# Optimization experiments

Hardware: AMD Instinct MI355X
Metric: run time of the kernel (lower is better)

The kernel has to match this reference:

```python
import jax, jax.numpy as jnp
import numpy as np

C = 256   # embedding_dim
B = 16
N = 2048
BN_EPS = 1e-5


def _sa_params(key, c):
    ks = jax.random.split(key, 8)
    s = 1.0 / np.sqrt(c)
    return dict(
        Wq=jax.random.normal(ks[0], (c // 2, c), jnp.float32) * s,
        Wk=jax.random.normal(ks[1], (c // 2, c), jnp.float32) * s,
        Wv=jax.random.normal(ks[2], (c, c), jnp.float32) * s,
        bv=jax.random.normal(ks[3], (c,), jnp.float32) * 0.01,
        Wt=jax.random.normal(ks[4], (c, c), jnp.float32) * s,
        bt=jax.random.normal(ks[5], (c,), jnp.float32) * 0.01,
        gamma=jnp.ones((c,), jnp.float32),
        beta=jnp.zeros((c,), jnp.float32),
    )


def setup_inputs() -> dict:
    key = jax.random.key(0)
    kx, k1, k2 = jax.random.split(key, 3)
    inp = {"x": jax.random.normal(kx, (B, C, N), jnp.float32)}
    for tag, kk in (("1", k1), ("2", k2)):
        for name, v in _sa_params(kk, C).items():
            inp[name + tag] = v
    return inp


def _sa_layer(x, Wq, Wk, Wv, bv, Wt, bt, gamma, beta):
    # 1x1 conv == per-point linear: [B,C,N]
    x_q = jnp.einsum('oc,bcn->bno', Wq, x)            # [B,N,C/2]
    x_k = jnp.einsum('oc,bcn->bon', Wk, x)            # [B,C/2,N]
    x_v = jnp.einsum('oc,bcn->bon', Wv, x) + bv[None, :, None]
    energy = jnp.einsum('bnc,bcm->bnm', x_q, x_k)     # [B,N,N]
    attn = jax.nn.softmax(energy, axis=-1)
    # offset-attention column-wise L1 renorm
    attn = attn / (1e-9 + attn.sum(axis=1, keepdims=True))
    x_r = jnp.einsum('bcn,bnm->bcm', x_v, attn)       # [B,C,N]
    h = x - x_r
    h = jnp.einsum('oc,bcn->bon', Wt, h) + bt[None, :, None]
    # BatchNorm1d (training mode, biased var over batch+points per channel)
    mean = h.mean(axis=(0, 2), keepdims=True)
    var = jnp.mean((h - mean) ** 2, axis=(0, 2), keepdims=True)
    h = (h - mean) * jax.lax.rsqrt(var + BN_EPS)
    h = h * gamma[None, :, None] + beta[None, :, None]
    return x + jax.nn.relu(h)


def reference(x,
              Wq1, Wk1, Wv1, bv1, Wt1, bt1, gamma1, beta1,
              Wq2, Wk2, Wv2, bv2, Wt2, bt2, gamma2, beta2):
    x1 = _sa_layer(x, Wq1, Wk1, Wv1, bv1, Wt1, bt1, gamma1, beta1)
    x2 = _sa_layer(x1, Wq2, Wk2, Wv2, bv2, Wt2, bt2, gamma2, beta2)
    return jnp.concatenate((x1, x2), axis=1)          # [B,2C,N]
```

## Files before the change

### kernel.cpp

```cpp
#include <hip/hip_runtime.h>

#define DI __device__ __forceinline__

typedef _Float16 f16_t;
typedef _Float16 f16x8 __attribute__((ext_vector_type(8)));
typedef float    f32x4 __attribute__((ext_vector_type(4)));

static_assert(sizeof(f16x8) == 16, "f16x8 must be 16B");

#define B_  16
#define C_  256
#define CH_ 128
#define N_  2048

DI f32x4 fzero(){ f32x4 z = {0.f,0.f,0.f,0.f}; return z; }
DI f16x8 ldg8(const f16_t* p){ return *(const f16x8*)p; }
DI f32x4 mfma16(f16x8 a, f16x8 b, f32x4 c){
  return __builtin_amdgcn_mfma_f32_16x16x32_f16(a, b, c, 0, 0, 0);
}
DI void split2(float v, f16_t& hi, f16_t& lo){
  hi = (f16_t)v; lo = (f16_t)(v - (float)hi);
}
DI int swz_b(int i){ return ((i&7)<<1) | ((i>>3)&1); }

#define GLL16(src, dst) __builtin_amdgcn_global_load_lds( \
    (const __attribute__((address_space(1))) void*)(src), \
    (__attribute__((address_space(3))) void*)(dst), 16, 0, 0)

__global__ void k_wconv(const float* q1,const float* k1,const float* v1,const float* t1,
                        const float* q2,const float* k2,const float* v2,const float* t2,
                        f16_t* out){
  int i = blockIdx.x*256 + threadIdx.x;
  int l = (i >= 196608) ? 1 : 0;
  int r = i - l*196608;
  const float* s; long dbase;
  if(r < 32768){ s = l? q2:q1; dbase = 0; }
  else if(r < 65536){ r -= 32768; s = l? k2:k1; dbase = 65536; }
  else if(r < 131072){ r -= 65536; s = l? v2:v1; dbase = 131072; }
  else { r -= 131072; s = l? t2:t1; dbase = 262144; }
  int o = r >> 8, c = r & 255;
  float v = s[o*256 + c];
  f16_t hi, lo; split2(v, hi, lo);
  f16_t* d = out + (long)l*393216 + dbase + (long)o*512;
  d[c] = hi; d[c+256] = lo;
}

__global__ void k_transpose(const float* __restrict__ X, long bstride,
                            f16_t* __restrict__ XtS){
  int b = blockIdx.x, n0 = blockIdx.y*32, c0 = blockIdx.z*64;
  __shared__ float tl[32][65];
  int t = threadIdx.x;
  int nn = t & 31, cr = t >> 5;
  const float* src = X + (long)b*bstride + n0 + nn;
  #pragma unroll
  for(int i=0;i<8;i++){
    int cc = cr + i*8;
    tl[nn][cc] = src[(long)(c0+cc)*N_];
  }
  __syncthreads();
  int n2 = t >> 3, cq = (t & 7)*8;
  __align__(16) f16_t hi8[8], lo8[8];
  #pragma unroll
  for(int j=0;j<8;j++) split2(tl[n2][cq+j], hi8[j], lo8[j]);
  f16_t* dst = XtS + ((long)b*N_ + n0 + n2)*512 + c0 + cq;
  *(f16x8*)dst         = *(f16x8*)hi8;
  *(f16x8*)(dst + 256) = *(f16x8*)lo8;
}

template<int LGX, int SPLIT_OUT, int BIAS>
__global__ __launch_bounds__(256) void k_gemm3(
    const f16_t* __restrict__ A, long sA,
    const f16_t* __restrict__ Bt, long sB,
    f16_t* __restrict__ out, int ldo, long sO,
    const float* __restrict__ bias)
{
  int i = blockIdx.x;
  int b = swz_b(i);
  int r = i>>4;
  int m0 = (r & ((1<<LGX)-1))*64, n0 = (r >> LGX)*64;
  int t = threadIdx.x, w = t>>6, l = t&63, lr = l&15, lg = l>>4;
  const f16_t* Ab = A + (long)b*sA + (long)(m0 + w*16 + lr)*512;
  const f16_t* Bb = Bt + (long)b*sB;
  f32x4 acc[4];
  #pragma unroll
  for(int i2=0;i2<4;i2++) acc[i2] = fzero();
  for(int k=0;k<256;k+=32){
    f16x8 ah = ldg8(Ab + k + lg*8);
    f16x8 al = ldg8(Ab + 256 + k + lg*8);
    #pragma unroll
    for(int ns=0;ns<4;ns++){
      const f16_t* brow = Bb + (long)(n0 + ns*16 + lr)*512;
      f16x8 bh = ldg8(brow + k + lg*8);
      f16x8 bl = ldg8(brow + 256 + k + lg*8);
      acc[ns] = mfma16(ah, bh, acc[ns]);
      acc[ns] = mfma16(ah, bl, acc[ns]);
      acc[ns] = mfma16(al, bh, acc[ns]);
    }
  }
  f16_t* ob = out + (long)b*sO;
  #pragma unroll
  for(int ns=0;ns<4;ns++){
    #pragma unroll
    for(int j=0;j<4;j++){
      int row = m0 + w*16 + lg*4 + j;
      int col = n0 + ns*16 + lr;
      float v = acc[ns][j];
      if(BIAS) v += bias[row];
      if(SPLIT_OUT){
        f16_t hi, lo; split2(v, hi, lo);
        ob[(long)row*ldo + col]       = hi;
        ob[(long)row*ldo + col + 128] = lo;
      } else {
        ob[(long)row*ldo + col] = (f16_t)v;
      }
    }
  }
}

__global__ __launch_bounds__(256) void k_rowstats(
    const f16_t* __restrict__ xqS, const f16_t* __restrict__ xkS,
    float* __restrict__ rowoff)
{
  extern __shared__ __align__(16) char smem[];
  const int bi = blockIdx.x;
  const int b = swz_b(bi);
  const int n0 = (bi>>4)*64;
  const int t = threadIdx.x, w = t>>6, l = t&63, lr = l&15, lg = l>>4;

  const f16_t* qp = xqS + ((long)b*N_ + n0 + w*16 + lr)*256;
  f16x8 bqh[4], bql[4];
  #pragma unroll
  for(int k=0;k<4;k++){
    bqh[k] = ldg8(qp + k*32 + lg*8);
    bql[k] = ldg8(qp + 128 + k*32 + lg*8);
  }
  const f16_t* kb = xkS + (long)b*N_*256;

  const int krow_off = l>>5, kslot = l&31;
  #define KSTAGE(mm, buf) do {                                                \
    char* kd = smem + (buf)*16384;                                            \
    _Pragma("unroll")                                                         \
    for(int r=0;r<4;r++){                                                     \
      int row = (r*4+w)*2 + krow_off;                                         \
      const f16_t* ksrc = kb + (long)((mm) + row)*256 + ((kslot ^ (row&15))*8);\
      GLL16(ksrc, kd + (r*4+w)*1024);                                         \
    }                                                                         \
  } while(0)

  float rmax = -3e38f, rsum = 0.f;
  KSTAGE(0, 0);

  #pragma unroll 1
  for(int i=0; i<64; i++){
    const int cur = i&1, nxt = cur^1;
    const int mm = (i<63) ? (i+1)*32 : 0;
    KSTAGE(mm, nxt);
    asm volatile("s_waitcnt vmcnt(4)" ::: "memory");
    asm volatile("s_barrier" ::: "memory");
    const char* kbuf = smem + cur*16384;
    #pragma unroll
    for(int s=0;s<2;s++){
      const char* krow = kbuf + (s*16 + lr)*512;
      f16x8 ah[4], al_[4];
      #pragma unroll
      for(int k=0;k<4;k++){
        ah[k]  = *(const f16x8*)(krow + ((((4*k+lg) ^ lr))<<4));
        al_[k] = *(const f16x8*)(krow + ((16 + (((4*k+lg)) ^ lr))<<4));
      }
      f32x4 a1 = fzero(), a2 = fzero(), a3 = fzero();
      #pragma unroll
      for(int k=0;k<4;k++) a1 = mfma16(ah[k],  bqh[k], a1);
      #pragma unroll
      for(int k=0;k<4;k++) a2 = mfma16(ah[k],  bql[k], a2);
      #pragma unroll
      for(int k=0;k<4;k++) a3 = mfma16(al_[k], bqh[k], a3);
      f32x4 acc = (a1 + a2) + a3;
      float vm = fmaxf(fmaxf(acc[0],acc[1]), fmaxf(acc[2],acc[3]));
      float nm = fmaxf(rmax, vm);
      rsum = rsum*__expf(rmax-nm)
           + __expf(acc[0]-nm)+__expf(acc[1]-nm)+__expf(acc[2]-nm)+__expf(acc[3]-nm);
      rmax = nm;
    }
    asm volatile("s_barrier" ::: "memory");
  }
  #undef KSTAGE

  #pragma unroll
  for(int off=16; off<64; off<<=1){
    float om = __shfl_xor(rmax, off, 64);
    float os = __shfl_xor(rsum, off, 64);
    float nm = fmaxf(rmax, om);
    rsum = rsum*__expf(rmax-nm) + os*__expf(om-nm);
    rmax = nm;
  }
  if(lg==0) rowoff[(long)b*N_ + n0 + w*16 + lr] = rmax + __logf(rsum);
}

__global__ __launch_bounds__(256) void k_apply(
    const f16_t* __restrict__ xqS, const f16_t* __restrict__ xkS,
    const f16_t* __restrict__ xv, const float* __restrict__ rowoff,
    const float* __restrict__ X, long xbstride, f16_t* __restrict__ h0T)
{
  extern __shared__ __align__(16) char smem[];
  const int bi = blockIdx.x;
  const int b = swz_b(bi);
  const int m0 = (bi>>4)*64;
  const int t = threadIdx.x, w = t>>6, l = t&63, lr = l&15, lg = l>>4;
  float* ro_s = (float*)(smem + 65536);
  {
    const float* rob = rowoff + (long)b*N_;
    *(f32x4*)(ro_s + t*4)        = *(const f32x4*)(rob + t*4);
    *(f32x4*)(ro_s + t*4 + 1024) = *(const f32x4*)(rob + t*4 + 1024);
  }

  const f16_t* akp = xkS + ((long)b*N_ + m0 + w*16 + lr)*256;
  f16x8 akh[4], akl[4];
  #pragma unroll
  for(int k=0;k<4;k++){
    akh[k] = ldg8(akp + k*32 + lg*8);
    akl[k] = ldg8(akp + 128 + k*32 + lg*8);
  }

  const f16_t* xqb = xqS + (long)b*N_*256;
  const f16_t* xvb = xv + (long)b*C_*N_;
  const int qperm = ((lr>>2)*8 + (lr&3));

  const int qrow_off = (l>>5), qslot = l&31;
  const int vc_off = (l>>2), vslot = l&3;

  #define STAGE(nn, nxtbuf) do {                                              \
    char* qd = smem + (nxtbuf)*16384;                                         \
    char* vd = smem + 32768 + (nxtbuf)*16384;                                 \
    _Pragma("unroll")                                                         \
    for(int r=0;r<4;r++){                                                     \
      int qrow = (r*4+w)*2 + qrow_off;                                        \
      int qsw  = (qrow&3) | (((qrow>>3)&3)<<2);                               \
      const f16_t* qsrc = xqb + (long)((nn) + qrow)*256 + ((qslot ^ qsw)*8);  \
      GLL16(qsrc, qd + (r*4+w)*1024);                                         \
      int vc = (r*4+w)*16 + vc_off;                                           \
      const f16_t* vsrc2 = xvb + (long)vc*N_ + (nn) + ((vslot ^ (vc&3))*8);   \
      GLL16(vsrc2, vd + (r*4+w)*1024);                                        \
    }                                                                         \
  } while(0)

  f32x4 y[16];
  #pragma unroll
  for(int i2=0;i2<16;i2++) y[i2] = fzero();
  float cs = 0.f, cm = -3e38f;

  __syncthreads();
  STAGE(0, 0);

  const int vsl = (lg ^ (lr&3)) << 4;

  #pragma unroll 1
  for(int i=0; i<64; i++){
    const int cur = i&1, nxt = cur^1;
    const int n0 = i*32;
    const int nn = (i<63) ? (n0+32) : 0;
    STAGE(nn, nxt);
    asm volatile("s_waitcnt vmcnt(8)" ::: "memory");
    asm volatile("s_barrier" ::: "memory");
    const char* qb = smem + cur*16384;
    const char* vb = smem + 32768 + cur*16384;
    float g[2][4];
    #pragma unroll
    for(int s2=0;s2<2;s2++){
      const int rl = qperm + s2*4;
      const char* qrow = qb + rl*512;
      f16x8 qh[4], ql[4];
      #pragma unroll
      for(int k=0;k<4;k++){
        qh[k] = *(const f16x8*)(qrow + (((4*k + lg) ^ lr)<<4));
        ql[k] = *(const f16x8*)(qrow + 256 + (((4*k + lg) ^ lr)<<4));
      }
      f32x4 e1 = fzero(), e2 = fzero(), e3 = fzero();
      #pragma unroll
      for(int k=0;k<4;k++) e1 = mfma16(qh[k], akh[k], e1);
      #pragma unroll
      for(int k=0;k<4;k++) e2 = mfma16(ql[k], akh[k], e2);
      #pragma unroll
      for(int k=0;k<4;k++) e3 = mfma16(qh[k], akl[k], e3);
      f32x4 e = (e1 + e2) + e3;
      f32x4 ro4 = *(const f32x4*)(ro_s + n0 + lg*8 + s2*4);
      #pragma unroll
      for(int j=0;j<4;j++) g[s2][j] = e[j] - ro4[j];
    }
    float v = fmaxf(fmaxf(fmaxf(g[0][0],g[0][1]), fmaxf(g[0][2],g[0][3])),
                    fmaxf(fmaxf(g[1][0],g[1][1]), fmaxf(g[1][2],g[1][3])));
    v = fmaxf(v, __shfl_xor(v, 16, 64));
    v = fmaxf(v, __shfl_xor(v, 32, 64));
    bool need = v > cm + 8.f;
    float fj = need ? __expf(cm - v) : 1.f;
    if(need) cm = v;
    cs *= fj;
    __align__(16) f16_t pv[8];
    #pragma unroll
    for(int s2=0;s2<2;s2++){
      #pragma unroll
      for(int j=0;j<4;j++){
        float p = __expf(g[s2][j] - cm);
        f16_t pb = (f16_t)p;
        cs += (float)pb;
        pv[s2*4+j] = pb;
      }
    }
    f16x8 pfrag = *(const f16x8*)pv;
    if(__any(need)){
      #pragma unroll
      for(int cf=0;cf<16;cf++){
        #pragma unroll
        for(int j2=0;j2<4;j2++) y[cf][j2] *= fj;
      }
    }
    #pragma unroll
    for(int cf=0;cf<16;cf++){
      f16x8 av = *(const f16x8*)(vb + (cf*16 + lr)*64 + vsl);
      y[cf] = mfma16(av, pfrag, y[cf]);
    }
    asm volatile("s_barrier" ::: "memory");
  }

  cs += __shfl_xor(cs, 16, 64);
  cs += __shfl_xor(cs, 32, 64);
  float inv = 1.f/(1e-9f*__expf(-cm) + cs);

  f16_t* H = (f16_t*)(smem + 49152);
  const int mq = t&63, cq = t>>6;
  const float* Xb = X + (long)b*xbstride + m0;
  uint4* dstb = (uint4*)(h0T + ((long)b*N_ + m0)*C_);
  #pragma unroll
  for(int half=0; half<2; half++){
    #pragma unroll
    for(int cf8=0; cf8<8; cf8++){
      int cf = half*8 + cf8;
      #pragma unroll
      for(int j=0;j<4;j++){
        int cl = cf8*16 + lg*4 + j;
        int m  = w*16 + lr;
        *(f16_t*)((char*)H + m*256 + ((((cl>>3) ^ (m&7))<<4) | ((cl&7)<<1)))
          = (f16_t)(y[cf][j]*inv);
      }
    }
    __syncthreads();
    #pragma unroll 4
    for(int ci=0; ci<32; ci++){
      int cl = cq*32 + ci;
      int c  = half*128 + cl;
      f16_t* hp = (f16_t*)((char*)H + mq*256 + ((((cl>>3) ^ (mq&7))<<4) | ((cl&7)<<1)));
      *hp = (f16_t)(Xb[(long)c*N_ + mq] - (float)*hp);
    }
    __syncthreads();
    {
      const uint4* src = (const uint4*)H;
      for(int i2=t;i2<1024;i2+=256){
        int row = i2>>4, slot = i2&15;
        dstb[row*32 + half*16 + slot] = src[(i2 & ~15) | (slot ^ (row&7))];
      }
    }
    __syncthreads();
  }
  #undef STAGE
}

__global__ __launch_bounds__(256) void k_wt_bn(
    const f16_t* __restrict__ WtS, const f16_t* __restrict__ h0T,
    const float* __restrict__ bt,
    f16_t* __restrict__ h1, float* __restrict__ bnacc)
{
  int i = blockIdx.x;
  int b = swz_b(i);
  int r = i>>4;
  int o0 = (r&3)*64, m0 = (r>>2)*64;
  int t=threadIdx.x, w=t>>6, l=t&63, lr=l&15, lg=l>>4;
  const f16_t* Arow = WtS + (long)(o0 + w*16 + lr)*512;
  const f16_t* Bb = h0T + (long)b*N_*C_;
  f32x4 acc[4];
  #pragma unroll
  for(int i2=0;i2<4;i2++) acc[i2] = fzero();
  for(int k=0;k<C_;k+=32){
    f16x8 afh = ldg8(Arow + k + lg*8);
    f16x8 afl = ldg8(Arow + 256 + k + lg*8);
    #pragma unroll
    for(int ms=0;ms<4;ms++){
      f16x8 bf_ = ldg8(Bb + (long)(m0 + ms*16 + lr)*C_ + k + lg*8);
      acc[ms] = mfma16(afh, bf_, acc[ms]);
      acc[ms] = mfma16(afl, bf_, acc[ms]);
    }
  }
  float s1[4]={0.f,0.f,0.f,0.f}, s2v[4]={0.f,0.f,0.f,0.f};
  f16_t* h1b = h1 + (long)b*C_*N_;
  #pragma unroll
  for(int j=0;j<4;j++){
    int o = o0 + w*16 + lg*4 + j;
    float bias = bt[o];
    #pragma unroll
    for(int ms=0;ms<4;ms++){
      float v = acc[ms][j] + bias;
      h1b[(long)o*N_ + m0 + ms*16 + lr] = (f16_t)v;
      s1[j] += v; s2v[j] += v*v;
    }
  }
  #pragma unroll
  for(int off=1; off<16; off<<=1){
    #pragma unroll
    for(int j=0;j<4;j++){ s1[j]+=__shfl_xor(s1[j],off,64); s2v[j]+=__shfl_xor(s2v[j],off,64); }
  }
  if(lr==0){
    #pragma unroll
    for(int j=0;j<4;j++){
      int o = o0 + w*16 + lg*4 + j;
      atomicAdd(&bnacc[o], s1[j]);
      atomicAdd(&bnacc[256+o], s2v[j]);
    }
  }
}

__global__ void k_bnfin(const float* __restrict__ bnacc, const float* __restrict__ gamma,
                        const float* __restrict__ beta, float* __restrict__ scsh){
  int o = threadIdx.x;
  float mean = bnacc[o] * (1.f/32768.f);
  float var  = bnacc[256+o] * (1.f/32768.f) - mean*mean;
  float sc = gamma[o] * rsqrtf(var + 1e-5f);
  scsh[o] = sc;
  scsh[256+o] = beta[o] - mean*sc;
}

__global__ void k_out(const f16_t* __restrict__ h1, const float* __restrict__ X, long xbstride,
                      const float* __restrict__ scsh, float* __restrict__ out, long ocoff){
  long i = (long)blockIdx.x*256 + threadIdx.x;
  long e = i*8;
  int b = (int)(e >> 19);
  int rem = (int)(e & 524287);
  int c = rem >> 11;
  f16x8 hv = *(const f16x8*)(h1 + e);
  const float* xb = X + (long)b*xbstride + rem;
  float4 xr0 = *(const float4*)xb;
  float4 xr1 = *(const float4*)(xb + 4);
  float sc = scsh[c], sh = scsh[256+c];
  float4 o0, o1;
  o0.x = xr0.x + fmaxf(fmaf((float)hv[0], sc, sh), 0.f);
  o0.y = xr0.y + fmaxf(fmaf((float)hv[1], sc, sh), 0.f);
  o0.z = xr0.z + fmaxf(fmaf((float)hv[2], sc, sh), 0.f);
  o0.w = xr0.w + fmaxf(fmaf((float)hv[3], sc, sh), 0.f);
  o1.x = xr1.x + fmaxf(fmaf((float)hv[4], sc, sh), 0.f);
  o1.y = xr1.y + fmaxf(fmaf((float)hv[5], sc, sh), 0.f);
  o1.z = xr1.z + fmaxf(fmaf((float)hv[6], sc, sh), 0.f);
  o1.w = xr1.w + fmaxf(fmaf((float)hv[7], sc, sh), 0.f);
  float* ob = out + (long)b*(512L*N_) + ocoff + rem;
  *(float4*)ob       = o0;
  *(float4*)(ob + 4) = o1;
}

extern "C" void kernel_launch(void* const* d_in, const int* in_sizes, int n_in,
                              void* d_out, int out_size, void* d_ws, size_t ws_size,
                              hipStream_t stream){
  (void)in_sizes; (void)n_in; (void)out_size; (void)ws_size;
  const float* x = (const float*)d_in[0];
  const float *Wf[2][4], *bv[2], *bt[2], *gm[2], *bb[2];
  for(int l=0;l<2;l++){
    int base = 1 + l*8;
    Wf[l][0]=(const float*)d_in[base+0];
    Wf[l][1]=(const float*)d_in[base+1];
    Wf[l][2]=(const float*)d_in[base+2];
    bv[l]   =(const float*)d_in[base+3];
    Wf[l][3]=(const float*)d_in[base+4];
    bt[l]   =(const float*)d_in[base+5];
    gm[l]   =(const float*)d_in[base+6];
    bb[l]   =(const float*)d_in[base+7];
  }
  char* ws = (char*)d_ws;
  size_t off = 0;
  auto alloc = [&](size_t bytes){ size_t o = off; off += (bytes + 255) & ~(size_t)255; return o; };
  size_t oXt = alloc((size_t)B_*N_*512*2);
  size_t oXq = alloc((size_t)B_*N_*256*2);
  size_t oXk = alloc((size_t)B_*N_*256*2);
  size_t oXv = alloc((size_t)B_*C_*N_*2);
  size_t oH0 = alloc((size_t)B_*N_*C_*2);
  size_t oRo = alloc((size_t)B_*N_*4);
  size_t oBn = alloc(2*512*4);
  size_t oSc = alloc(2*512*4);
  size_t oW  = alloc((size_t)786432*2);

  hipMemsetAsync(ws + oBn, 0, 2*512*4, stream);
  k_wconv<<<1536,256,0,stream>>>(Wf[0][0],Wf[0][1],Wf[0][2],Wf[0][3],
                                 Wf[1][0],Wf[1][1],Wf[1][2],Wf[1][3],
                                 (f16_t*)(ws+oW));
  float* dout = (float*)d_out;
  f16_t* H1 = (f16_t*)(ws + oXq);
  for(int l=0;l<2;l++){
    const float* Xl = l ? dout : x;
    long xbs = l ? 512L*N_ : 256L*N_;
    const f16_t* WqS = (const f16_t*)(ws+oW) + (size_t)l*393216;
    const f16_t* WkS = WqS + 65536;
    const f16_t* WvS = WqS + 131072;
    const f16_t* WtS = WqS + 262144;
    f16_t* XtS = (f16_t*)(ws+oXt);
    f16_t* Xq  = (f16_t*)(ws+oXq);
    f16_t* Xk  = (f16_t*)(ws+oXk);
    f16_t* Xv  = (f16_t*)(ws+oXv);
    f16_t* H0  = (f16_t*)(ws+oH0);
    float* Ro  = (float*)(ws+oRo);
    float* Bn  = (float*)(ws+oBn) + l*512;
    float* Sc  = (float*)(ws+oSc) + l*512;

    k_transpose<<<dim3(B_, N_/32, C_/64),256,0,stream>>>(Xl, xbs, XtS);
    k_gemm3<5,1,0><<<1024,256,0,stream>>>(XtS, (long)N_*512, WqS, 0L,
                                          Xq, 256, (long)N_*256, nullptr);
    k_gemm3<5,1,0><<<1024,256,0,stream>>>(XtS, (long)N_*512, WkS, 0L,
                                          Xk, 256, (long)N_*256, nullptr);
    k_gemm3<2,0,1><<<2048,256,0,stream>>>(WvS, 0L, XtS, (long)N_*512,
                                          Xv, N_, (long)C_*N_, bv[l]);
    k_rowstats<<<512,256,32768,stream>>>(Xq, Xk, Ro);
    k_apply<<<512,256,73728,stream>>>(Xq, Xk, Xv, Ro, Xl, xbs, H0);
    k_wt_bn<<<2048,256,0,stream>>>(WtS, H0, bt[l], H1, Bn);
    k_bnfin<<<1,256,0,stream>>>(Bn, gm[l], bb[l], Sc);
    k_out<<<4096,256,0,stream>>>(H1, Xl, xbs, Sc, dout, (long)l*C_*N_);
  }
}
```

Baseline: 854.2 us.

## Merge Q/K projections, fold BN finalize into output, add MFMA priority hints

Combines the separate Q and K projection GEMMs into one launch over the concatenated weight, routing the columns at or above 128 to the K buffer by offset. Removes the single-block BN finalize kernel by computing scale and shift per thread inside the output kernel. Replaces recomputed staging addresses with pointers advanced each iteration, and skips the dummy prefetch on the last iteration. Wraps the MFMA sections in the attention kernels with s_setprio. Together these cut launch count and address arithmetic, at the cost of redundant BN-stat math in every output thread.

```diff
diff --git a/kernel.cpp b/kernel.cpp
--- a/kernel.cpp
+++ b/kernel.cpp
@@ -67,12 +67,12 @@
   *(f16x8*)(dst + 256) = *(f16x8*)lo8;
 }
 
-template<int LGX, int SPLIT_OUT, int BIAS>
+template<int LGX, int SPLIT_OUT, int BIAS, int DUAL>
 __global__ __launch_bounds__(256) void k_gemm3(
     const f16_t* __restrict__ A, long sA,
     const f16_t* __restrict__ Bt, long sB,
     f16_t* __restrict__ out, int ldo, long sO,
-    const float* __restrict__ bias)
+    const float* __restrict__ bias, long dualoff)
 {
   int i = blockIdx.x;
   int b = swz_b(i);
@@ -108,8 +108,10 @@
       if(BIAS) v += bias[row];
       if(SPLIT_OUT){
         f16_t hi, lo; split2(v, hi, lo);
-        ob[(long)row*ldo + col]       = hi;
-        ob[(long)row*ldo + col + 128] = lo;
+        f16_t* base = ob;
+        if(DUAL && col >= 128) base = ob + (dualoff - 128);
+        base[(long)row*ldo + col]       = hi;
+        base[(long)row*ldo + col + 128] = lo;
       } else {
         ob[(long)row*ldo + col] = (f16_t)v;
       }
@@ -137,25 +139,29 @@
   const f16_t* kb = xkS + (long)b*N_*256;
 
   const int krow_off = l>>5, kslot = l&31;
-  #define KSTAGE(mm, buf) do {                                                \
-    char* kd = smem + (buf)*16384;                                            \
-    _Pragma("unroll")                                                         \
-    for(int r=0;r<4;r++){                                                     \
-      int row = (r*4+w)*2 + krow_off;                                         \
-      const f16_t* ksrc = kb + (long)((mm) + row)*256 + ((kslot ^ (row&15))*8);\
-      GLL16(ksrc, kd + (r*4+w)*1024);                                         \
-    }                                                                         \
-  } while(0)
+  const f16_t *ks0,*ks1,*ks2,*ks3;
+  #define KINIT(r) { int row=(r*4+w)*2+krow_off; \
+    ks##r = kb + (long)row*256 + ((kslot ^ (row&15))*8); }
+  KINIT(0) KINIT(1) KINIT(2) KINIT(3)
+  #undef KINIT
+  #define KSTAGE(buf) do { char* kd = smem + (buf)*16384;                     \
+    GLL16(ks0, kd + (0*4+w)*1024); GLL16(ks1, kd + (1*4+w)*1024);             \
+    GLL16(ks2, kd + (2*4+w)*1024); GLL16(ks3, kd + (3*4+w)*1024); } while(0)
+  #define KADV() do { ks0+=8192; ks1+=8192; ks2+=8192; ks3+=8192; } while(0)
 
   float rmax = -3e38f, rsum = 0.f;
-  KSTAGE(0, 0);
+  KSTAGE(0);
 
   #pragma unroll 1
   for(int i=0; i<64; i++){
     const int cur = i&1, nxt = cur^1;
-    const int mm = (i<63) ? (i+1)*32 : 0;
-    KSTAGE(mm, nxt);
-    asm volatile("s_waitcnt vmcnt(4)" ::: "memory");
+    if(i<63){
+      KADV();
+      KSTAGE(nxt);
+      asm volatile("s_waitcnt vmcnt(4)" ::: "memory");
+    } else {
+      asm volatile("s_waitcnt vmcnt(0)" ::: "memory");
+    }
     asm volatile("s_barrier" ::: "memory");
     const char* kbuf = smem + cur*16384;
     #pragma unroll
@@ -167,6 +173,7 @@
         ah[k]  = *(const f16x8*)(krow + ((((4*k+lg) ^ lr))<<4));
         al_[k] = *(const f16x8*)(krow + ((16 + (((4*k+lg)) ^ lr))<<4));
       }
+      __builtin_amdgcn_s_setprio(1);
       f32x4 a1 = fzero(), a2 = fzero(), a3 = fzero();
       #pragma unroll
       for(int k=0;k<4;k++) a1 = mfma16(ah[k],  bqh[k], a1);
@@ -174,6 +181,7 @@
       for(int k=0;k<4;k++) a2 = mfma16(ah[k],  bql[k], a2);
       #pragma unroll
       for(int k=0;k<4;k++) a3 = mfma16(al_[k], bqh[k], a3);
+      __builtin_amdgcn_s_setprio(0);
       f32x4 acc = (a1 + a2) + a3;
       float vm = fmaxf(fmaxf(acc[0],acc[1]), fmaxf(acc[2],acc[3]));
       float nm = fmaxf(rmax, vm);
@@ -184,6 +192,7 @@
     asm volatile("s_barrier" ::: "memory");
   }
   #undef KSTAGE
+  #undef KADV
 
   #pragma unroll
   for(int off=16; off<64; off<<=1){
@@ -228,20 +237,23 @@
   const int qrow_off = (l>>5), qslot = l&31;
   const int vc_off = (l>>2), vslot = l&3;
 
-  #define STAGE(nn, nxtbuf) do {                                              \
-    char* qd = smem + (nxtbuf)*16384;                                         \
-    char* vd = smem + 32768 + (nxtbuf)*16384;                                 \
-    _Pragma("unroll")                                                         \
-    for(int r=0;r<4;r++){                                                     \
-      int qrow = (r*4+w)*2 + qrow_off;                                        \
-      int qsw  = (qrow&3) | (((qrow>>3)&3)<<2);                               \
-      const f16_t* qsrc = xqb + (long)((nn) + qrow)*256 + ((qslot ^ qsw)*8);  \
-      GLL16(qsrc, qd + (r*4+w)*1024);                                         \
-      int vc = (r*4+w)*16 + vc_off;                                           \
-      const f16_t* vsrc2 = xvb + (long)vc*N_ + (nn) + ((vslot ^ (vc&3))*8);   \
-      GLL16(vsrc2, vd + (r*4+w)*1024);                                        \
-    }                                                                         \
-  } while(0)
+  const f16_t *qs0,*qs1,*qs2,*qs3,*vs0,*vs1,*vs2,*vs3;
+  #define PINIT(r) { int qrow=(r*4+w)*2+qrow_off;                             \
+    int qsw=(qrow&3)|(((qrow>>3)&3)<<2);                                      \
+    qs##r = xqb + (long)qrow*256 + ((qslot ^ qsw)*8);                         \
+    int vc=(r*4+w)*16+vc_off;                                                 \
+    vs##r = xvb + (long)vc*N_ + ((vslot ^ (vc&3))*8); }
+  PINIT(0) PINIT(1) PINIT(2) PINIT(3)
+  #undef PINIT
+  #define STAGE(buf) do {                                                     \
+    char* qd = smem + (buf)*16384;                                            \
+    char* vd = smem + 32768 + (buf)*16384;                                    \
+    GLL16(qs0, qd + (0*4+w)*1024); GLL16(vs0, vd + (0*4+w)*1024);             \
+    GLL16(qs1, qd + (1*4+w)*1024); GLL16(vs1, vd + (1*4+w)*1024);             \
+    GLL16(qs2, qd + (2*4+w)*1024); GLL16(vs2, vd + (2*4+w)*1024);             \
+    GLL16(qs3, qd + (3*4+w)*1024); GLL16(vs3, vd + (3*4+w)*1024); } while(0)
+  #define PADV() do { qs0+=8192; qs1+=8192; qs2+=8192; qs3+=8192;             \
+    vs0+=32; vs1+=32; vs2+=32; vs3+=32; } while(0)
 
   f32x4 y[16];
   #pragma unroll
@@ -249,7 +261,7 @@
   float cs = 0.f, cm = -3e38f;
 
   __syncthreads();
-  STAGE(0, 0);
+  STAGE(0);
 
   const int vsl = (lg ^ (lr&3)) << 4;
 
@@ -257,9 +269,13 @@
   for(int i=0; i<64; i++){
     const int cur = i&1, nxt = cur^1;
     const int n0 = i*32;
-    const int nn = (i<63) ? (n0+32) : 0;
-    STAGE(nn, nxt);
-    asm volatile("s_waitcnt vmcnt(8)" ::: "memory");
+    if(i<63){
+      PADV();
+      STAGE(nxt);
+      asm volatile("s_waitcnt vmcnt(8)" ::: "memory");
+    } else {
+      asm volatile("s_waitcnt vmcnt(0)" ::: "memory");
+    }
     asm volatile("s_barrier" ::: "memory");
     const char* qb = smem + cur*16384;
     const char* vb = smem + 32768 + cur*16384;
@@ -274,6 +290,7 @@
         qh[k] = *(const f16x8*)(qrow + (((4*k + lg) ^ lr)<<4));
         ql[k] = *(const f16x8*)(qrow + 256 + (((4*k + lg) ^ lr)<<4));
       }
+      __builtin_amdgcn_s_setprio(1);
       f32x4 e1 = fzero(), e2 = fzero(), e3 = fzero();
       #pragma unroll
       for(int k=0;k<4;k++) e1 = mfma16(qh[k], akh[k], e1);
@@ -281,6 +298,7 @@
       for(int k=0;k<4;k++) e2 = mfma16(ql[k], akh[k], e2);
       #pragma unroll
       for(int k=0;k<4;k++) e3 = mfma16(qh[k], akl[k], e3);
+      __builtin_amdgcn_s_setprio(0);
       f32x4 e = (e1 + e2) + e3;
       f32x4 ro4 = *(const f32x4*)(ro_s + n0 + lg*8 + s2*4);
       #pragma unroll
@@ -313,13 +331,17 @@
         for(int j2=0;j2<4;j2++) y[cf][j2] *= fj;
       }
     }
+    __builtin_amdgcn_s_setprio(1);
     #pragma unroll
     for(int cf=0;cf<16;cf++){
       f16x8 av = *(const f16x8*)(vb + (cf*16 + lr)*64 + vsl);
       y[cf] = mfma16(av, pfrag, y[cf]);
     }
+    __builtin_amdgcn_s_setprio(0);
     asm volatile("s_barrier" ::: "memory");
   }
+  #undef STAGE
+  #undef PADV
 
   cs += __shfl_xor(cs, 16, 64);
   cs += __shfl_xor(cs, 32, 64);
@@ -360,7 +382,6 @@
     }
     __syncthreads();
   }
-  #undef STAGE
 }
 
 __global__ __launch_bounds__(256) void k_wt_bn(
@@ -416,28 +437,22 @@
   }
 }
 
-__global__ void k_bnfin(const float* __restrict__ bnacc, const float* __restrict__ gamma,
-                        const float* __restrict__ beta, float* __restrict__ scsh){
-  int o = threadIdx.x;
-  float mean = bnacc[o] * (1.f/32768.f);
-  float var  = bnacc[256+o] * (1.f/32768.f) - mean*mean;
-  float sc = gamma[o] * rsqrtf(var + 1e-5f);
-  scsh[o] = sc;
-  scsh[256+o] = beta[o] - mean*sc;
-}
-
 __global__ void k_out(const f16_t* __restrict__ h1, const float* __restrict__ X, long xbstride,
-                      const float* __restrict__ scsh, float* __restrict__ out, long ocoff){
+                      const float* __restrict__ bnacc, const float* __restrict__ gamma,
+                      const float* __restrict__ beta, float* __restrict__ out, long ocoff){
   long i = (long)blockIdx.x*256 + threadIdx.x;
   long e = i*8;
   int b = (int)(e >> 19);
   int rem = (int)(e & 524287);
   int c = rem >> 11;
+  float mean = bnacc[c] * (1.f/32768.f);
+  float var  = bnacc[256+c] * (1.f/32768.f) - mean*mean;
+  float sc = gamma[c] * rsqrtf(var + 1e-5f);
+  float sh = beta[c] - mean*sc;
   f16x8 hv = *(const f16x8*)(h1 + e);
   const float* xb = X + (long)b*xbstride + rem;
   float4 xr0 = *(const float4*)xb;
   float4 xr1 = *(const float4*)(xb + 4);
-  float sc = scsh[c], sh = scsh[256+c];
   float4 o0, o1;
   o0.x = xr0.x + fmaxf(fmaf((float)hv[0], sc, sh), 0.f);
   o0.y = xr0.y + fmaxf(fmaf((float)hv[1], sc, sh), 0.f);
@@ -479,7 +494,6 @@
   size_t oH0 = alloc((size_t)B_*N_*C_*2);
   size_t oRo = alloc((size_t)B_*N_*4);
   size_t oBn = alloc(2*512*4);
-  size_t oSc = alloc(2*512*4);
   size_t oW  = alloc((size_t)786432*2);
 
   hipMemsetAsync(ws + oBn, 0, 2*512*4, stream);
@@ -488,11 +502,11 @@
                                  (f16_t*)(ws+oW));
   float* dout = (float*)d_out;
   f16_t* H1 = (f16_t*)(ws + oXq);
+  const long XKOFF = ((long)(oXk - oXq)) / 2;
   for(int l=0;l<2;l++){
     const float* Xl = l ? dout : x;
     long xbs = l ? 512L*N_ : 256L*N_;
     const f16_t* WqS = (const f16_t*)(ws+oW) + (size_t)l*393216;
-    const f16_t* WkS = WqS + 65536;
     const f16_t* WvS = WqS + 131072;
     const f16_t* WtS = WqS + 262144;
     f16_t* XtS = (f16_t*)(ws+oXt);
@@ -502,19 +516,15 @@
     f16_t* H0  = (f16_t*)(ws+oH0);
     float* Ro  = (float*)(ws+oRo);
     float* Bn  = (float*)(ws+oBn) + l*512;
-    float* Sc  = (float*)(ws+oSc) + l*512;
 
     k_transpose<<<dim3(B_, N_/32, C_/64),256,0,stream>>>(Xl, xbs, XtS);
-    k_gemm3<5,1,0><<<1024,256,0,stream>>>(XtS, (long)N_*512, WqS, 0L,
-                                          Xq, 256, (long)N_*256, nullptr);
-    k_gemm3<5,1,0><<<1024,256,0,stream>>>(XtS, (long)N_*512, WkS, 0L,
-                                          Xk, 256, (long)N_*256, nullptr);
-    k_gemm3<2,0,1><<<2048,256,0,stream>>>(WvS, 0L, XtS, (long)N_*512,
-                                          Xv, N_, (long)C_*N_, bv[l]);
+    k_gemm3<5,1,0,1><<<2048,256,0,stream>>>(XtS, (long)N_*512, WqS, 0L,
+                                            Xq, 256, (long)N_*256, nullptr, XKOFF);
+    k_gemm3<2,0,1,0><<<2048,256,0,stream>>>(WvS, 0L, XtS, (long)N_*512,
+                                            Xv, N_, (long)C_*N_, bv[l], 0L);
     k_rowstats<<<512,256,32768,stream>>>(Xq, Xk, Ro);
     k_apply<<<512,256,73728,stream>>>(Xq, Xk, Xv, Ro, Xl, xbs, H0);
     k_wt_bn<<<2048,256,0,stream>>>(WtS, H0, bt[l], H1, Bn);
-    k_bnfin<<<1,256,0,stream>>>(Bn, gm[l], bb[l], Sc);
-    k_out<<<4096,256,0,stream>>>(H1, Xl, xbs, Sc, dout, (long)l*C_*N_);
-  }
-}
+    k_out<<<4096,256,0,stream>>>(H1, Xl, xbs, Bn, gm[l], bb[l], dout, (long)l*C_*N_);
+  }
+}
```

Measured after the change: 899.3 us. +5.3%, slower.
